# Kernel tuning notes

Measured on AMD Instinct MI355X. Metric: run time of the kernel, lower is better.

## Reference

```python
import jax, jax.numpy as jnp
import numpy as np

BN_EPS = 1e-5


def _conv2d(x, w, pad):
    # x: [B,C,H,W], w: [O,I,kh,kw]
    return jax.lax.conv_general_dilated(
        x, w, window_strides=(1, 1), padding=((pad, pad), (pad, pad)),
        dimension_numbers=("NCHW", "OIHW", "NCHW"))


def _feat(x, conv_w, bn_gamma, bn_beta, bn_mean, bn_var, desc_w, desc_b):
    # BasicConv(64->32, k=3, pad=1): conv (no bias) -> BN (inference) -> ReLU
    y = _conv2d(x, conv_w, pad=1)
    inv = bn_gamma / jnp.sqrt(bn_var + BN_EPS)
    y = y * inv[None, :, None, None] + (bn_beta - bn_mean * inv)[None, :, None, None]
    y = jnp.maximum(y, 0.0)
    # desc: 1x1 conv 32->32 with bias
    y = _conv2d(y, desc_w, pad=0) + desc_b[None, :, None, None]
    return y  # [B,32,H,W]


def setup_inputs() -> dict:
    key = jax.random.key(0)
    ks = jax.random.split(key, 4)
    B, Cin, H, W = 8, 64, 160, 576
    left = jax.random.normal(ks[0], (B, Cin, H, W), dtype=jnp.float32)
    right = jax.random.normal(ks[1], (B, Cin, H, W), dtype=jnp.float32)
    conv_w = jax.random.normal(ks[2], (32, 64, 3, 3), dtype=jnp.float32) * 0.05
    bn_gamma = jnp.ones((32,), jnp.float32)
    bn_beta = jnp.zeros((32,), jnp.float32)
    bn_mean = jnp.zeros((32,), jnp.float32)
    bn_var = jnp.ones((32,), jnp.float32)
    desc_w = jax.random.normal(ks[3], (32, 32, 1, 1), dtype=jnp.float32) * 0.1
    desc_b = jnp.zeros((32,), jnp.float32)
    return {"left": left, "right": right, "conv_w": conv_w,
            "bn_gamma": bn_gamma, "bn_beta": bn_beta,
            "bn_mean": bn_mean, "bn_var": bn_var,
            "desc_w": desc_w, "desc_b": desc_b, "maxdisp": 48}


def reference(left, right, conv_w, bn_gamma, bn_beta, bn_mean, bn_var,
              desc_w, desc_b, maxdisp):
    L = _feat(left, conv_w, bn_gamma, bn_beta, bn_mean, bn_var, desc_w, desc_b)
    R = _feat(right, conv_w, bn_gamma, bn_beta, bn_mean, bn_var, desc_w, desc_b)
    # reduce_mean is a frozen 1x1 conv with weight 1/32 == mean over channels.
    cv = [jnp.mean(L * R, axis=1)]  # d = 0, [B,H,W]
    for d in range(1, maxdisp):  # maxdisp is a static Python int (structural)
        c = jnp.mean(L[:, :, :, d:] * R[:, :, :, :-d], axis=1)  # [B,H,W-d]
        cv.append(jnp.pad(c, ((0, 0), (0, 0), (d, 0))))  # zero-pad left edge
    return jnp.stack(cv, axis=1)  # [B, maxdisp, H, W]
```

## Files before the change

### kernel.cpp

```cpp
#include <hip/hip_runtime.h>
#include <stdint.h>

#define HH   160
#define WW   576
#define CIN  64
#define BATCH 8
#define MAXD 48

typedef unsigned int  uint;
typedef unsigned short ushort;
typedef __attribute__((ext_vector_type(8))) short bf16x8;
typedef __attribute__((ext_vector_type(4))) float f32x4;

static constexpr size_t WTB_OFF  = 0;
static constexpr size_t DWT_OFF  = 36864;
static constexpr size_t B1_OFF   = 38912;
static constexpr size_t B2_OFF   = 39040;
static constexpr size_t FEAT_OFF = 40960;
static constexpr size_t FEAT_ELEMS = (size_t)BATCH * HH * WW * 32;

__device__ __forceinline__ uint f2bf(float f) {
    uint u = __float_as_uint(f);
    u = (u + 0x7fffu + ((u >> 16) & 1u)) >> 16;
    return u;
}
__device__ __forceinline__ float bf2f_lo(uint u) { return __uint_as_float(u << 16); }
__device__ __forceinline__ float bf2f_hi(uint u) { return __uint_as_float(u & 0xffff0000u); }
__device__ __forceinline__ uint pk2(float a, float b) { return f2bf(a) | (f2bf(b) << 16); }

__global__ void prep_kernel(const float* __restrict__ conv_w,
                            const float* __restrict__ gamma,
                            const float* __restrict__ beta,
                            const float* __restrict__ mean,
                            const float* __restrict__ var,
                            const float* __restrict__ desc_w,
                            const float* __restrict__ desc_b,
                            char* __restrict__ ws) {
    int tid = blockIdx.x * 256 + threadIdx.x;
    ushort* wtB = (ushort*)(ws + WTB_OFF);
    ushort* dwt = (ushort*)(ws + DWT_OFF);
    float*  b1  = (float*)(ws + B1_OFF);
    float*  b2  = (float*)(ws + B2_OFF);
    if (tid < 36 * 64 * 8) {
        int j    = tid & 7;
        int lane = (tid >> 3) & 63;
        int frag = tid >> 9;
        int ln = lane & 15, g = lane >> 4;
        int mt  = frag & 1;
        int kk  = (frag >> 1) & 1;
        int tap = frag >> 2;
        int ch = mt * 16 + ln;
        int ci = kk * 32 + g * 8 + j;
        float inv = gamma[ch] * rsqrtf(var[ch] + 1e-5f);
        wtB[tid] = (ushort)f2bf(conv_w[(size_t)(ch * 64 + ci) * 9 + tap] * inv);
    }
    if (tid < 1024) {
        int o = tid >> 5, p = tid & 31;
        int g = p >> 3, j = p & 7;
        int mid = 4 * g + (j & 3) + 16 * ((j >> 2) & 1);
        dwt[tid] = (ushort)f2bf(desc_w[o * 32 + mid]);
    }
    if (tid < 32) {
        float inv = gamma[tid] * rsqrtf(var[tid] + 1e-5f);
        b1[tid] = beta[tid] - mean[tid] * inv;
        b2[tid] = desc_b[tid];
    }
}

#define NXB 9
#define NYB 40
#define NWG (NXB * NYB * 2 * BATCH)
__global__ __launch_bounds__(512, 4)
void feat_mfma(const float* __restrict__ left,
               const float* __restrict__ right,
               const char* __restrict__ ws,
               ushort* __restrict__ featL,
               ushort* __restrict__ featR) {
    __shared__ __align__(16) ushort tile[6 * 72 * 64];

    int bid = blockIdx.x;
    int nid = (bid & 7) * (NWG / 8) + (bid >> 3);
    int x    = nid % NXB;
    int rest = nid / NXB;
    int hy   = rest % NYB;
    int z    = rest / NYB;
    int b    = z & 7;
    const float* __restrict__ in = (z < 8 ? left : right) + (size_t)b * CIN * HH * WW;
    ushort* __restrict__ feat = (z < 8 ? featL : featR);
    const int w0 = x * 64;
    const int h0 = hy * 4;
    const int PL = HH * WW;

    for (int t = threadIdx.x; t < 6 * 8 * 18; t += 512) {
        int g    = t % 18;
        int rest2 = t / 18;
        int oct  = rest2 & 7;
        int r    = rest2 >> 3;
        int gh  = h0 + r - 1;
        int gw4 = w0 - 4 + g * 4;
        float4 v[8];
        if (((unsigned)gh < HH) && ((unsigned)gw4 < WW)) {
            const float* src = in + (size_t)(oct * 8) * PL + (size_t)gh * WW + gw4;
#pragma unroll
            for (int j = 0; j < 8; ++j)
                v[j] = *(const float4*)(src + (size_t)j * PL);
        } else {
#pragma unroll
            for (int j = 0; j < 8; ++j) v[j] = make_float4(0.f, 0.f, 0.f, 0.f);
        }
#pragma unroll
        for (int k = 0; k < 4; ++k) {
            float w_[8] = {k == 0 ? v[0].x : k == 1 ? v[0].y : k == 2 ? v[0].z : v[0].w,
                           k == 0 ? v[1].x : k == 1 ? v[1].y : k == 2 ? v[1].z : v[1].w,
                           k == 0 ? v[2].x : k == 1 ? v[2].y : k == 2 ? v[2].z : v[2].w,
                           k == 0 ? v[3].x : k == 1 ? v[3].y : k == 2 ? v[3].z : v[3].w,
                           k == 0 ? v[4].x : k == 1 ? v[4].y : k == 2 ? v[4].z : v[4].w,
                           k == 0 ? v[5].x : k == 1 ? v[5].y : k == 2 ? v[5].z : v[5].w,
                           k == 0 ? v[6].x : k == 1 ? v[6].y : k == 2 ? v[6].z : v[6].w,
                           k == 0 ? v[7].x : k == 1 ? v[7].y : k == 2 ? v[7].z : v[7].w};
            uint4 o;
            o.x = pk2(w_[0], w_[1]);
            o.y = pk2(w_[2], w_[3]);
            o.z = pk2(w_[4], w_[5]);
            o.w = pk2(w_[6], w_[7]);
            int px = r * 72 + g * 4 + k;
            *(uint4*)&tile[(size_t)px * 64 + ((oct ^ (px & 7)) * 8)] = o;
        }
    }
    __syncthreads();

    const int lane = threadIdx.x & 63;
    const int wv   = threadIdx.x >> 6;
    const int ln   = lane & 15;
    const int g    = lane >> 4;
    const int orow = wv >> 1;
    const int ocol = (wv & 1) * 32;

    const ushort* __restrict__ wtB = (const ushort*)(ws + WTB_OFF);

    f32x4 acc[2][2] = {};

#pragma unroll
    for (int tap = 0; tap < 9; ++tap) {
        const int r = tap / 3, kw = tap % 3;
#pragma unroll
        for (int kk = 0; kk < 2; ++kk) {
            bf16x8 a0 = *(const bf16x8*)(wtB + (size_t)((tap * 2 + kk) * 2 + 0) * 512 + lane * 8);
            bf16x8 a1 = *(const bf16x8*)(wtB + (size_t)((tap * 2 + kk) * 2 + 1) * 512 + lane * 8);
            bf16x8 bb[2];
#pragma unroll
            for (int nt = 0; nt < 2; ++nt) {
                int px = (orow + r) * 72 + ocol + nt * 16 + ln + kw + 3;
                bb[nt] = *(const bf16x8*)&tile[(size_t)px * 64 + (((kk * 4 + g) ^ (px & 7)) * 8)];
            }
            acc[0][0] = __builtin_amdgcn_mfma_f32_16x16x32_bf16(a0, bb[0], acc[0][0], 0, 0, 0);
            acc[0][1] = __builtin_amdgcn_mfma_f32_16x16x32_bf16(a0, bb[1], acc[0][1], 0, 0, 0);
            acc[1][0] = __builtin_amdgcn_mfma_f32_16x16x32_bf16(a1, bb[0], acc[1][0], 0, 0, 0);
            acc[1][1] = __builtin_amdgcn_mfma_f32_16x16x32_bf16(a1, bb[1], acc[1][1], 0, 0, 0);
        }
    }

    const float* __restrict__ b1 = (const float*)(ws + B1_OFF);
    const float* __restrict__ b2 = (const float*)(ws + B2_OFF);
    f32x4 b1v0 = *(const f32x4*)(b1 + g * 4);
    f32x4 b1v1 = *(const f32x4*)(b1 + 16 + g * 4);
    bf16x8 p[2];
#pragma unroll
    for (int nt = 0; nt < 2; ++nt) {
#pragma unroll
        for (int j = 0; j < 8; ++j) {
            float v = acc[j >> 2][nt][j & 3] + ((j >> 2) ? b1v1[j & 3] : b1v0[j & 3]);
            v = fmaxf(v, 0.f);
            p[nt][j] = (short)f2bf(v);
        }
    }

    const ushort* __restrict__ dwt = (const ushort*)(ws + DWT_OFF);
    const ushort* dBase = dwt + ln * 32 + g * 8;
    bf16x8 da0 = *(const bf16x8*)(dBase);
    bf16x8 da1 = *(const bf16x8*)(dBase + 512);
    f32x4 b2v0 = *(const f32x4*)(b2 + g * 4);
    f32x4 b2v1 = *(const f32x4*)(b2 + 16 + g * 4);
    f32x4 acc2[2][2];
#pragma unroll
    for (int nt = 0; nt < 2; ++nt) { acc2[0][nt] = b2v0; acc2[1][nt] = b2v1; }
#pragma unroll
    for (int nt = 0; nt < 2; ++nt) {
        acc2[0][nt] = __builtin_amdgcn_mfma_f32_16x16x32_bf16(da0, p[nt], acc2[0][nt], 0, 0, 0);
        acc2[1][nt] = __builtin_amdgcn_mfma_f32_16x16x32_bf16(da1, p[nt], acc2[1][nt], 0, 0, 0);
    }

    size_t pixBase = ((size_t)b * HH + h0 + orow) * WW + w0 + ocol + ln;
#pragma unroll
    for (int nt = 0; nt < 2; ++nt) {
#pragma unroll
        for (int mt2 = 0; mt2 < 2; ++mt2) {
            uint u0 = f2bf(acc2[mt2][nt][0]) | (f2bf(acc2[mt2][nt][1]) << 16);
            uint u1 = f2bf(acc2[mt2][nt][2]) | (f2bf(acc2[mt2][nt][3]) << 16);
            *(uint2*)(feat + (pixBase + nt * 16) * 32 + mt2 * 16 + g * 4) = make_uint2(u0, u1);
        }
    }
}

#define CVT 192
__global__ __launch_bounds__(CVT)
void cv_kernel(const ushort* __restrict__ featL,
               const ushort* __restrict__ featR,
               float* __restrict__ out) {
    __shared__ ushort r_lds[WW * 40];

    const int t  = threadIdx.x;
    const int bh = blockIdx.x;
    const int b  = bh / HH;
    const int h  = bh - b * HH;
    const ushort* __restrict__ Lrow = featL + ((size_t)b * HH + h) * WW * 32;
    const ushort* __restrict__ Rrow = featR + ((size_t)b * HH + h) * WW * 32;

#pragma unroll
    for (int k = 0; k < 3; ++k) {
        int w = t + k * CVT;
        const uint4* src = (const uint4*)(Rrow + (size_t)w * 32);
        uint4* dst = (uint4*)(r_lds + (size_t)w * 40);
#pragma unroll
        for (int j = 0; j < 4; ++j) dst[j] = src[j];
    }

    float Lf[3][32];
#pragma unroll
    for (int k = 0; k < 3; ++k) {
        int w = t + k * CVT;
        const uint4* src = (const uint4*)(Lrow + (size_t)w * 32);
#pragma unroll
        for (int j = 0; j < 4; ++j) {
            uint4 v = src[j];
            uint vv[4] = {v.x, v.y, v.z, v.w};
#pragma unroll
            for (int q = 0; q < 4; ++q) {
                Lf[k][j * 8 + q * 2]     = bf2f_lo(vv[q]);
                Lf[k][j * 8 + q * 2 + 1] = bf2f_hi(vv[q]);
            }
        }
    }
    __syncthreads();

    float* __restrict__ outBase = out + ((size_t)b * MAXD * HH + h) * WW;
    for (int d = 0; d < MAXD; ++d) {
#pragma unroll
        for (int k = 0; k < 3; ++k) {
            int w = t + k * CVT;
            float res = 0.f;
            if (w >= d) {
                const uint4* rp = (const uint4*)(r_lds + (size_t)(w - d) * 40);
                float s0 = 0.f, s1 = 0.f;
#pragma unroll
                for (int j = 0; j < 4; ++j) {
                    uint4 v = rp[j];
                    uint vv[4] = {v.x, v.y, v.z, v.w};
#pragma unroll
                    for (int q = 0; q < 4; ++q) {
                        int idx = j * 8 + q * 2;
                        s0 = fmaf(Lf[k][idx],     bf2f_lo(vv[q]), s0);
                        s1 = fmaf(Lf[k][idx + 1], bf2f_hi(vv[q]), s1);
                    }
                }
                res = (s0 + s1) * (1.f / 32.f);
            }
            outBase[(size_t)d * HH * WW + w] = res;
        }
    }
}

extern "C" void kernel_launch(void* const* d_in, const int* in_sizes, int n_in,
                              void* d_out, int out_size, void* d_ws, size_t ws_size,
                              hipStream_t stream) {
    const float* left   = (const float*)d_in[0];
    const float* right  = (const float*)d_in[1];
    const float* conv_w = (const float*)d_in[2];
    const float* gamma  = (const float*)d_in[3];
    const float* beta   = (const float*)d_in[4];
    const float* mean   = (const float*)d_in[5];
    const float* var    = (const float*)d_in[6];
    const float* desc_w = (const float*)d_in[7];
    const float* desc_b = (const float*)d_in[8];
    float*  out   = (float*)d_out;
    char*   ws    = (char*)d_ws;
    ushort* featL = (ushort*)(ws + FEAT_OFF);
    ushort* featR = featL + FEAT_ELEMS;

    prep_kernel<<<72, 256, 0, stream>>>(conv_w, gamma, beta, mean, var, desc_w, desc_b, ws);
    feat_mfma<<<NWG, 512, 0, stream>>>(left, right, ws, featL, featR);
    cv_kernel<<<BATCH * HH, CVT, 0, stream>>>(featL, featR, out);
}
```

Measured before the change: 254.1 us.

## Switch feature conv to 32x32x16 MFMA with narrower 32-wide tiles

Moves the 3x3 conv and the 1x1 descriptor GEMM from 16x16x32 to 32x32x16 bf16 MFMA instructions, with the prep kernel re-laying out the weight fragments to match. Workgroups shrink to 256 threads covering 32 columns by 4 rows, so the grid doubles and the LDS tile drops to 222 pixels. The load loop now skips halo columns that are not needed. The aim is fewer MFMA and LDS fragment loads per output and better occupancy, at the cost of more halo reloading per output column, since tiles are narrower.

```diff
diff --git a/kernel.cpp b/kernel.cpp
--- a/kernel.cpp
+++ b/kernel.cpp
@@ -11,6 +11,7 @@
 typedef unsigned short ushort;
 typedef __attribute__((ext_vector_type(8))) short bf16x8;
 typedef __attribute__((ext_vector_type(4))) float f32x4;
+typedef __attribute__((ext_vector_type(16))) float f32x16;
 
 static constexpr size_t WTB_OFF  = 0;
 static constexpr size_t DWT_OFF  = 36864;
@@ -27,6 +28,9 @@
 __device__ __forceinline__ float bf2f_lo(uint u) { return __uint_as_float(u << 16); }
 __device__ __forceinline__ float bf2f_hi(uint u) { return __uint_as_float(u & 0xffff0000u); }
 __device__ __forceinline__ uint pk2(float a, float b) { return f2bf(a) | (f2bf(b) << 16); }
+__device__ __forceinline__ float elem4(float4 f, int k) {
+    return k == 0 ? f.x : k == 1 ? f.y : k == 2 ? f.z : f.w;
+}
 
 __global__ void prep_kernel(const float* __restrict__ conv_w,
                             const float* __restrict__ gamma,
@@ -43,21 +47,21 @@
     float*  b2  = (float*)(ws + B2_OFF);
     if (tid < 36 * 64 * 8) {
         int j    = tid & 7;
-        int lane = (tid >> 3) & 63;
-        int frag = tid >> 9;
-        int ln = lane & 15, g = lane >> 4;
-        int mt  = frag & 1;
-        int kk  = (frag >> 1) & 1;
-        int tap = frag >> 2;
-        int ch = mt * 16 + ln;
-        int ci = kk * 32 + g * 8 + j;
+        int l    = (tid >> 3) & 63;
+        int f    = tid >> 9;
+        int s    = f & 3;
+        int tap  = f >> 2;
+        int ch = l & 31;
+        int ci = s * 16 + (l >> 5) * 8 + j;
         float inv = gamma[ch] * rsqrtf(var[ch] + 1e-5f);
         wtB[tid] = (ushort)f2bf(conv_w[(size_t)(ch * 64 + ci) * 9 + tap] * inv);
     }
     if (tid < 1024) {
-        int o = tid >> 5, p = tid & 31;
-        int g = p >> 3, j = p & 7;
-        int mid = 4 * g + (j & 3) + 16 * ((j >> 2) & 1);
+        int j = tid & 7;
+        int l = (tid >> 3) & 63;
+        int s = tid >> 9;
+        int o = l & 31;
+        int mid = (j & 3) + 8 * (j >> 2) + 16 * s + 4 * (l >> 5);
         dwt[tid] = (ushort)f2bf(desc_w[o * 32 + mid]);
     }
     if (tid < 32) {
@@ -67,16 +71,16 @@
     }
 }
 
-#define NXB 9
+#define NXB 18
 #define NYB 40
 #define NWG (NXB * NYB * 2 * BATCH)
-__global__ __launch_bounds__(512, 4)
+__global__ __launch_bounds__(256, 5)
 void feat_mfma(const float* __restrict__ left,
                const float* __restrict__ right,
                const char* __restrict__ ws,
                ushort* __restrict__ featL,
                ushort* __restrict__ featR) {
-    __shared__ __align__(16) ushort tile[6 * 72 * 64];
+    __shared__ __align__(16) ushort tile[222 * 64];
 
     int bid = blockIdx.x;
     int nid = (bid & 7) * (NWG / 8) + (bid >> 3);
@@ -87,15 +91,15 @@
     int b    = z & 7;
     const float* __restrict__ in = (z < 8 ? left : right) + (size_t)b * CIN * HH * WW;
     ushort* __restrict__ feat = (z < 8 ? featL : featR);
-    const int w0 = x * 64;
+    const int w0 = x * 32;
     const int h0 = hy * 4;
     const int PL = HH * WW;
 
-    for (int t = threadIdx.x; t < 6 * 8 * 18; t += 512) {
-        int g    = t % 18;
-        int rest2 = t / 18;
-        int oct  = rest2 & 7;
-        int r    = rest2 >> 3;
+    for (int t = threadIdx.x; t < 6 * 10 * 8; t += 256) {
+        int oct = t & 7;
+        int rem = t >> 3;
+        int g   = rem % 10;
+        int r   = rem / 10;
         int gh  = h0 + r - 1;
         int gw4 = w0 - 4 + g * 4;
         float4 v[8];
@@ -110,95 +114,74 @@
         }
 #pragma unroll
         for (int k = 0; k < 4; ++k) {
-            float w_[8] = {k == 0 ? v[0].x : k == 1 ? v[0].y : k == 2 ? v[0].z : v[0].w,
-                           k == 0 ? v[1].x : k == 1 ? v[1].y : k == 2 ? v[1].z : v[1].w,
-                           k == 0 ? v[2].x : k == 1 ? v[2].y : k == 2 ? v[2].z : v[2].w,
-                           k == 0 ? v[3].x : k == 1 ? v[3].y : k == 2 ? v[3].z : v[3].w,
-                           k == 0 ? v[4].x : k == 1 ? v[4].y : k == 2 ? v[4].z : v[4].w,
-                           k == 0 ? v[5].x : k == 1 ? v[5].y : k == 2 ? v[5].z : v[5].w,
-                           k == 0 ? v[6].x : k == 1 ? v[6].y : k == 2 ? v[6].z : v[6].w,
-                           k == 0 ? v[7].x : k == 1 ? v[7].y : k == 2 ? v[7].z : v[7].w};
-            uint4 o;
-            o.x = pk2(w_[0], w_[1]);
-            o.y = pk2(w_[2], w_[3]);
-            o.z = pk2(w_[4], w_[5]);
-            o.w = pk2(w_[6], w_[7]);
-            int px = r * 72 + g * 4 + k;
-            *(uint4*)&tile[(size_t)px * 64 + ((oct ^ (px & 7)) * 8)] = o;
+            int c = g * 4 + k;
+            if (c < 3 || c > 36) continue;
+            uint4 o4;
+            o4.x = pk2(elem4(v[0], k), elem4(v[1], k));
+            o4.y = pk2(elem4(v[2], k), elem4(v[3], k));
+            o4.z = pk2(elem4(v[4], k), elem4(v[5], k));
+            o4.w = pk2(elem4(v[6], k), elem4(v[7], k));
+            int px = r * 37 + c;
+            *(uint4*)&tile[(size_t)px * 64 + ((oct ^ (px & 7)) * 8)] = o4;
         }
     }
     __syncthreads();
 
     const int lane = threadIdx.x & 63;
     const int wv   = threadIdx.x >> 6;
-    const int ln   = lane & 15;
-    const int g    = lane >> 4;
-    const int orow = wv >> 1;
-    const int ocol = (wv & 1) * 32;
+    const int n    = lane & 31;
+    const int hi   = lane >> 5;
 
     const ushort* __restrict__ wtB = (const ushort*)(ws + WTB_OFF);
 
-    f32x4 acc[2][2] = {};
-
+    f32x16 acc = {};
 #pragma unroll
     for (int tap = 0; tap < 9; ++tap) {
         const int r = tap / 3, kw = tap % 3;
-#pragma unroll
-        for (int kk = 0; kk < 2; ++kk) {
-            bf16x8 a0 = *(const bf16x8*)(wtB + (size_t)((tap * 2 + kk) * 2 + 0) * 512 + lane * 8);
-            bf16x8 a1 = *(const bf16x8*)(wtB + (size_t)((tap * 2 + kk) * 2 + 1) * 512 + lane * 8);
-            bf16x8 bb[2];
-#pragma unroll
-            for (int nt = 0; nt < 2; ++nt) {
-                int px = (orow + r) * 72 + ocol + nt * 16 + ln + kw + 3;
-                bb[nt] = *(const bf16x8*)&tile[(size_t)px * 64 + (((kk * 4 + g) ^ (px & 7)) * 8)];
-            }
-            acc[0][0] = __builtin_amdgcn_mfma_f32_16x16x32_bf16(a0, bb[0], acc[0][0], 0, 0, 0);
-            acc[0][1] = __builtin_amdgcn_mfma_f32_16x16x32_bf16(a0, bb[1], acc[0][1], 0, 0, 0);
-            acc[1][0] = __builtin_amdgcn_mfma_f32_16x16x32_bf16(a1, bb[0], acc[1][0], 0, 0, 0);
-            acc[1][1] = __builtin_amdgcn_mfma_f32_16x16x32_bf16(a1, bb[1], acc[1][1], 0, 0, 0);
+        const int px = (wv + r) * 37 + n + kw + 3;
+        const ushort* bbase = &tile[(size_t)px * 64];
+        const int ph = px & 7;
+#pragma unroll
+        for (int s = 0; s < 4; ++s) {
+            bf16x8 a  = *(const bf16x8*)(wtB + (size_t)((tap * 4 + s) * 64 + lane) * 8);
+            bf16x8 bb = *(const bf16x8*)(bbase + (((2 * s + hi) ^ ph) * 8));
+            acc = __builtin_amdgcn_mfma_f32_32x32x16_bf16(a, bb, acc, 0, 0, 0);
         }
     }
 
     const float* __restrict__ b1 = (const float*)(ws + B1_OFF);
     const float* __restrict__ b2 = (const float*)(ws + B2_OFF);
-    f32x4 b1v0 = *(const f32x4*)(b1 + g * 4);
-    f32x4 b1v1 = *(const f32x4*)(b1 + 16 + g * 4);
-    bf16x8 p[2];
-#pragma unroll
-    for (int nt = 0; nt < 2; ++nt) {
-#pragma unroll
-        for (int j = 0; j < 8; ++j) {
-            float v = acc[j >> 2][nt][j & 3] + ((j >> 2) ? b1v1[j & 3] : b1v0[j & 3]);
-            v = fmaxf(v, 0.f);
-            p[nt][j] = (short)f2bf(v);
-        }
+    f32x4 b1q[4], b2q[4];
+#pragma unroll
+    for (int q = 0; q < 4; ++q) {
+        b1q[q] = *(const f32x4*)(b1 + 8 * q + 4 * hi);
+        b2q[q] = *(const f32x4*)(b2 + 8 * q + 4 * hi);
+    }
+    bf16x8 p0, p1;
+#pragma unroll
+    for (int j = 0; j < 8; ++j) {
+        float v0 = fmaxf(acc[j]     + b1q[j >> 2][j & 3],       0.f);
+        float v1 = fmaxf(acc[8 + j] + b1q[2 + (j >> 2)][j & 3], 0.f);
+        p0[j] = (short)f2bf(v0);
+        p1[j] = (short)f2bf(v1);
     }
 
     const ushort* __restrict__ dwt = (const ushort*)(ws + DWT_OFF);
-    const ushort* dBase = dwt + ln * 32 + g * 8;
-    bf16x8 da0 = *(const bf16x8*)(dBase);
-    bf16x8 da1 = *(const bf16x8*)(dBase + 512);
-    f32x4 b2v0 = *(const f32x4*)(b2 + g * 4);
-    f32x4 b2v1 = *(const f32x4*)(b2 + 16 + g * 4);
-    f32x4 acc2[2][2];
-#pragma unroll
-    for (int nt = 0; nt < 2; ++nt) { acc2[0][nt] = b2v0; acc2[1][nt] = b2v1; }
-#pragma unroll
-    for (int nt = 0; nt < 2; ++nt) {
-        acc2[0][nt] = __builtin_amdgcn_mfma_f32_16x16x32_bf16(da0, p[nt], acc2[0][nt], 0, 0, 0);
-        acc2[1][nt] = __builtin_amdgcn_mfma_f32_16x16x32_bf16(da1, p[nt], acc2[1][nt], 0, 0, 0);
-    }
-
-    size_t pixBase = ((size_t)b * HH + h0 + orow) * WW + w0 + ocol + ln;
-#pragma unroll
-    for (int nt = 0; nt < 2; ++nt) {
-#pragma unroll
-        for (int mt2 = 0; mt2 < 2; ++mt2) {
-            uint u0 = f2bf(acc2[mt2][nt][0]) | (f2bf(acc2[mt2][nt][1]) << 16);
-            uint u1 = f2bf(acc2[mt2][nt][2]) | (f2bf(acc2[mt2][nt][3]) << 16);
-            *(uint2*)(feat + (pixBase + nt * 16) * 32 + mt2 * 16 + g * 4) = make_uint2(u0, u1);
-        }
+    bf16x8 da0 = *(const bf16x8*)(dwt + (size_t)lane * 8);
+    bf16x8 da1 = *(const bf16x8*)(dwt + (size_t)(64 + lane) * 8);
+    f32x16 acc2;
+#pragma unroll
+    for (int j = 0; j < 16; ++j) acc2[j] = b2q[j >> 2][j & 3];
+    acc2 = __builtin_amdgcn_mfma_f32_32x32x16_bf16(da0, p0, acc2, 0, 0, 0);
+    acc2 = __builtin_amdgcn_mfma_f32_32x32x16_bf16(da1, p1, acc2, 0, 0, 0);
+
+    size_t pix = ((size_t)b * HH + h0 + wv) * WW + w0 + n;
+    ushort* fp = feat + pix * 32 + 4 * hi;
+#pragma unroll
+    for (int q = 0; q < 4; ++q) {
+        uint u0 = pk2(acc2[4 * q],     acc2[4 * q + 1]);
+        uint u1 = pk2(acc2[4 * q + 2], acc2[4 * q + 3]);
+        *(uint2*)(fp + 8 * q) = make_uint2(u0, u1);
     }
 }
 
@@ -288,6 +271,6 @@
     ushort* featR = featL + FEAT_ELEMS;
 
     prep_kernel<<<72, 256, 0, stream>>>(conv_w, gamma, beta, mean, var, desc_w, desc_b, ws);
-    feat_mfma<<<NWG, 512, 0, stream>>>(left, right, ws, featL, featR);
+    feat_mfma<<<NWG, 256, 0, stream>>>(left, right, ws, featL, featR);
     cv_kernel<<<BATCH * HH, CVT, 0, stream>>>(featL, featR, out);
 }
```

Result: slower. 306.7 us (+20.7%).
